# Performance work log

Measured on AMD Instinct MI355X. Metric: run time of the kernel, lower is better.

The kernel has to match this reference:

```python
import jax, jax.numpy as jnp
import numpy as np

N = 100000      # nodes
E = 1600000     # edges (avg degree 16)
IN = 128
OUT = 256


def setup_inputs() -> dict:
    key = jax.random.key(0)
    ks = jax.random.split(key, 8)
    x = jax.random.normal(ks[0], (N, IN), dtype=jnp.float32)
    edge_index = jax.random.randint(ks[1], (2, E), 0, N, dtype=jnp.int64)
    # GCNConv weights (glorot-ish scale) and biases
    W1 = jax.random.normal(ks[2], (IN, OUT), dtype=jnp.float32) / np.float32(np.sqrt(IN))
    b1 = jnp.zeros((OUT,), jnp.float32)
    W2 = jax.random.normal(ks[3], (OUT, OUT), dtype=jnp.float32) / np.float32(np.sqrt(OUT))
    b2 = jnp.zeros((OUT,), jnp.float32)
    # projection Linear(IN, OUT)
    Wp = jax.random.normal(ks[4], (IN, OUT), dtype=jnp.float32) / np.float32(np.sqrt(IN))
    bp = jax.random.normal(ks[5], (OUT,), dtype=jnp.float32) * 0.01
    return {"x": x, "edge_index": edge_index, "W1": W1, "b1": b1,
            "W2": W2, "b2": b2, "Wp": Wp, "bp": bp}


def _gcn_conv(x, W, b, src, dst, n):
    """PyG GCNConv: D^{-1/2}(A+I)D^{-1/2} X W + b. src/dst already include self-loops."""
    xw = x @ W                                              # [n, out]
    ones = jnp.ones(src.shape[0], dtype=xw.dtype)
    deg = jax.ops.segment_sum(ones, dst, num_segments=n)    # in-degree incl. self-loop
    dinv = jnp.where(deg > 0, jax.lax.rsqrt(deg), 0.0)
    norm = dinv[src] * dinv[dst]                            # [e]
    msgs = xw[src] * norm[:, None]                          # gather + scale
    out = jax.ops.segment_sum(msgs, dst, num_segments=n)    # scatter-add
    return out + b


def reference(x, edge_index, W1, b1, W2, b2, Wp, bp):
    n = x.shape[0]
    loop = jnp.arange(n, dtype=edge_index.dtype)            # self-loops
    src = jnp.concatenate([edge_index[0], loop])
    dst = jnp.concatenate([edge_index[1], loop])
    out = jax.nn.relu(_gcn_conv(x, W1, b1, src, dst, n))
    out = _gcn_conv(out, W2, b2, src, dst, n)
    identity = x @ Wp + bp                                  # projection (IN != OUT)
    return jax.nn.relu(out + identity)
```

## Files before the change

### kernel.cpp

```cpp
#include <hip/hip_runtime.h>

#define NODES 100000
#define EDGES 1600000
#define FIN   128
#define FOUT  256
#define NBUCK 196

typedef __bf16 bf16;
typedef __bf16 bf16x8 __attribute__((ext_vector_type(8)));
typedef __bf16 bf16x4 __attribute__((ext_vector_type(4)));
typedef __bf16 bf16x2 __attribute__((ext_vector_type(2)));
typedef float  f32x4  __attribute__((ext_vector_type(4)));
typedef float  f32x2  __attribute__((ext_vector_type(2)));

__device__ __forceinline__ f32x2 bf2f(unsigned w) {
    f32x2 r;
    r[0] = __uint_as_float(w << 16);
    r[1] = __uint_as_float(w & 0xffff0000u);
    return r;
}

__global__ __launch_bounds__(256) void detect_kernel(const void* __restrict__ x,
                                                     const int* __restrict__ ei,
                                                     int* __restrict__ flags) {
    __shared__ int s_f32_evidence;
    __shared__ int s_odd_nonzero;
    int t = threadIdx.x;
    if (t == 0) { s_f32_evidence = 0; s_odd_nonzero = 0; }
    __syncthreads();
    const bf16* xb = (const bf16*)x;
    int local_f32 = 0;
    for (int i = t; i < 4096; i += 256) {
        float v = fabsf((float)xb[i]);
        if (!(v < 1e4f)) local_f32 = 1;
    }
    if (local_f32) atomicOr(&s_f32_evidence, 1);
    int local_odd = 0;
    for (int k = t; k < 1024; k += 256) {
        if (ei[2 * k + 1] != 0) local_odd = 1;
    }
    if (local_odd) atomicOr(&s_odd_nonzero, 1);
    __syncthreads();
    if (t == 0) {
        flags[0] = s_f32_evidence ? 0 : 1;
        flags[1] = s_odd_nonzero ? 0 : 1;
    }
}

__device__ __forceinline__ int edge_at(const int* __restrict__ ei, int which, int i,
                                       int is64) {
    if (is64) return ei[2 * (which * EDGES + i)];
    return ei[which * EDGES + i];
}

__global__ __launch_bounds__(512) void deg_count(const int* __restrict__ ei,
                                                 int* __restrict__ deg,
                                                 int* __restrict__ bhist,
                                                 const int* __restrict__ flags) {
    __shared__ int lh[256];
    int t = threadIdx.x;
    if (t < 256) lh[t] = 0;
    __syncthreads();
    int i = blockIdx.x * 512 + t;
    if (i < EDGES) {
        int is64 = flags[1];
        int s = edge_at(ei, 0, i, is64);
        int d = edge_at(ei, 1, i, is64);
        if (s >= 0 && s < NODES && d >= 0 && d < NODES) {
            atomicAdd(&deg[d], 1);
            atomicAdd(&lh[d >> 9], 1);
        }
    }
    __syncthreads();
    if (t < NBUCK && lh[t] > 0) atomicAdd(&bhist[t], lh[t]);
}

__global__ __launch_bounds__(256) void deg_to_dinv(const int* __restrict__ deg,
                                                   float* __restrict__ dinv, int n) {
    int i = blockIdx.x * 256 + threadIdx.x;
    if (i < n) dinv[i] = rsqrtf((float)deg[i] + 1.0f);
}

__global__ __launch_bounds__(1024) void scan1(const int* __restrict__ deg,
                                              int* __restrict__ col_ptr,
                                              int* __restrict__ blksum, int n) {
    __shared__ int sm[1024];
    int t = threadIdx.x;
    int i = blockIdx.x * 1024 + t;
    int v = (i < n) ? deg[i] : 0;
    sm[t] = v;
    __syncthreads();
    for (int off = 1; off < 1024; off <<= 1) {
        int u = (t >= off) ? sm[t - off] : 0;
        __syncthreads();
        sm[t] += u;
        __syncthreads();
    }
    if (i <= n) col_ptr[i] = sm[t] - v;
    if (t == 1023) blksum[blockIdx.x] = sm[t];
}

__global__ __launch_bounds__(128) void scan2(int* blk, int nblk) {
    __shared__ int sm[128];
    int t = threadIdx.x;
    int v = (t < nblk) ? blk[t] : 0;
    sm[t] = v;
    __syncthreads();
    for (int off = 1; off < 128; off <<= 1) {
        int u = (t >= off) ? sm[t - off] : 0;
        __syncthreads();
        sm[t] += u;
        __syncthreads();
    }
    if (t < nblk) blk[t] = sm[t] - v;
}

__global__ __launch_bounds__(256) void scan3(int* __restrict__ col_ptr,
                                             const int* __restrict__ blkoff, int n) {
    int i = blockIdx.x * 256 + threadIdx.x;
    if (i <= n) col_ptr[i] += blkoff[i >> 10];
}

__global__ __launch_bounds__(256) void bucket_scan(const int* __restrict__ bhist,
                                                   int* __restrict__ bbase,
                                                   int* __restrict__ bcur) {
    __shared__ int sm[256];
    int t = threadIdx.x;
    int v = (t < NBUCK) ? bhist[t] : 0;
    sm[t] = v;
    __syncthreads();
    for (int off = 1; off < 256; off <<= 1) {
        int u = (t >= off) ? sm[t - off] : 0;
        __syncthreads();
        sm[t] += u;
        __syncthreads();
    }
    if (t < NBUCK) {
        int ex = sm[t] - v;
        bbase[t] = ex;
        bcur[t]  = ex;
        if (t == NBUCK - 1) bbase[NBUCK] = sm[t];
    }
}

#define EPB 4096
__global__ __launch_bounds__(256) void partition_edges(const int* __restrict__ ei,
                                                       int* __restrict__ bcur,
                                                       uint2* __restrict__ pairs,
                                                       const int* __restrict__ flags) {
    __shared__ int lh[256], sc[256], lst[256], lcu[256], gb[256];
    __shared__ uint2 stage[EPB];
    int t = threadIdx.x;
    int base = blockIdx.x * EPB;
    int is64 = flags[1];

    lh[t] = 0;
    __syncthreads();

    int es[16], ed[16];
#pragma unroll
    for (int j = 0; j < 16; ++j) {
        int i = base + j * 256 + t;
        int s = -1, d = -1;
        if (i < EDGES) {
            s = edge_at(ei, 0, i, is64);
            d = edge_at(ei, 1, i, is64);
            if (s < 0 || s >= NODES || d < 0 || d >= NODES) d = -1;
        }
        es[j] = s; ed[j] = d;
        if (d >= 0) atomicAdd(&lh[d >> 9], 1);
    }
    __syncthreads();
    sc[t] = lh[t];
    __syncthreads();
    for (int off = 1; off < 256; off <<= 1) {
        int u = (t >= off) ? sc[t - off] : 0;
        __syncthreads();
        sc[t] += u;
        __syncthreads();
    }
    int start = sc[t] - lh[t];
    lst[t] = start;
    lcu[t] = start;
    __syncthreads();
#pragma unroll
    for (int j = 0; j < 16; ++j) {
        if (ed[j] >= 0) {
            int p = atomicAdd(&lcu[ed[j] >> 9], 1);
            stage[p] = make_uint2((unsigned)es[j], (unsigned)ed[j]);
        }
    }
    __syncthreads();
    if (t < NBUCK && lh[t] > 0) gb[t] = atomicAdd(&bcur[t], lh[t]);
    __syncthreads();
    int nval = sc[255];
    for (int slot = t; slot < nval; slot += 256) {
        uint2 e = stage[slot];
        int b = (int)(e.y >> 9);
        pairs[(size_t)gb[b] + (slot - lst[b])] = e;
    }
}

__global__ __launch_bounds__(512) void fine_fill(const uint2* __restrict__ pairs,
                                                 const int* __restrict__ bbase,
                                                 const int* __restrict__ col_ptr,
                                                 int* __restrict__ col_idx) {
    __shared__ int lcur[512];
    int b = blockIdx.x;
    int t = threadIdx.x;
    int node = (b << 9) + t;
    lcur[t] = (node < NODES) ? col_ptr[node] : 0;
    __syncthreads();
    int beg = bbase[b], end = bbase[b + 1];
    for (int i = beg + t; i < end; i += 512) {
        uint2 e = pairs[i];
        int pos = atomicAdd(&lcur[e.y & 511], 1);
        col_idx[pos] = (int)e.x;
    }
}

__global__ __launch_bounds__(256) void pack_all(const void* __restrict__ W1,
                                                const void* __restrict__ W2,
                                                const void* __restrict__ Wp,
                                                const void* __restrict__ b1,
                                                const void* __restrict__ b2,
                                                const void* __restrict__ bp,
                                                bf16* __restrict__ W1p, bf16* __restrict__ W2p,
                                                bf16* __restrict__ Wpp, bf16* __restrict__ b1b,
                                                bf16* __restrict__ b2b, bf16* __restrict__ bpb,
                                                const int* __restrict__ flags) {
    int fl = flags[0];
    int b = blockIdx.x;
    if (b < 512) {
        const void* W; bf16* Wo; int idx;
        if (b < 128)      { W = W1; Wo = W1p; idx = b * 256 + threadIdx.x; }
        else if (b < 384) { W = W2; Wo = W2p; idx = (b - 128) * 256 + threadIdx.x; }
        else              { W = Wp; Wo = Wpp; idx = (b - 384) * 256 + threadIdx.x; }
        int j    = idx & 7;
        int lane = (idx >> 3) & 63;
        int ct   = (idx >> 9) & 15;
        int kt   = idx >> 13;
        int k = kt * 32 + (lane >> 4) * 8 + j;
        int n = ct * 16 + (lane & 15);
        Wo[idx] = fl ? ((const bf16*)W)[k * 256 + n]
                     : (bf16)(((const float*)W)[k * 256 + n]);
    } else {
        const void* bb; bf16* bo;
        if (b == 512)      { bb = b1; bo = b1b; }
        else if (b == 513) { bb = b2; bo = b2b; }
        else               { bb = bp; bo = bpb; }
        int i = threadIdx.x;
        bo[i] = fl ? ((const bf16*)bb)[i] : (bf16)(((const float*)bb)[i]);
    }
}

__global__ __launch_bounds__(256) void scale_x(const void* __restrict__ xv,
                                               const float* __restrict__ dinv,
                                               bf16* __restrict__ Xs,
                                               const int* __restrict__ flags) {
    int idx = blockIdx.x * 256 + threadIdx.x;
    if (idx >= NODES * 16) return;
    int row = idx >> 4, seg = idx & 15;
    float di = dinv[row];
    bf16x8 o;
    if (flags[0]) {
        bf16x8 v = *(const bf16x8*)((const bf16*)xv + (size_t)row * FIN + seg * 8);
#pragma unroll
        for (int j = 0; j < 8; ++j) o[j] = (bf16)(di * (float)v[j]);
    } else {
        const float* p = (const float*)xv + (size_t)row * FIN + seg * 8;
        f32x4 lo = *(const f32x4*)p;
        f32x4 hi = *(const f32x4*)(p + 4);
#pragma unroll
        for (int j = 0; j < 4; ++j) { o[j] = (bf16)(di * lo[j]); o[j + 4] = (bf16)(di * hi[j]); }
    }
    *(bf16x8*)(Xs + (size_t)row * FIN + seg * 8) = o;
}

__global__ __launch_bounds__(256) void gemm_proj(const void* __restrict__ Av,
                                                 const bf16* __restrict__ Wpk,
                                                 const bf16* __restrict__ bias,
                                                 bf16* __restrict__ projb,
                                                 const int* __restrict__ flags) {
    int a_f32 = (flags[0] == 0);
    int wave = threadIdx.x >> 6;
    int lane = threadIdx.x & 63;
    int row0 = blockIdx.x * 64;
    int lr = lane & 15;
    int lk = (lane >> 4) * 8;

    int arow[4];
#pragma unroll
    for (int rf = 0; rf < 4; ++rf) {
        int r = row0 + rf * 16 + lr;
        arow[rf] = r < NODES ? r : (NODES - 1);
    }

    f32x4 acc[4][4];
    f32x4 z = {0.f, 0.f, 0.f, 0.f};
#pragma unroll
    for (int i = 0; i < 4; ++i)
#pragma unroll
        for (int j = 0; j < 4; ++j) acc[i][j] = z;

    for (int kt = 0; kt < 4; ++kt) {
        bf16x8 af[4];
        if (!a_f32) {
            const bf16* Ab = (const bf16*)Av + kt * 32 + lk;
#pragma unroll
            for (int rf = 0; rf < 4; ++rf)
                af[rf] = *(const bf16x8*)(Ab + (size_t)arow[rf] * FIN);
        } else {
            const float* Af = (const float*)Av + kt * 32 + lk;
#pragma unroll
            for (int rf = 0; rf < 4; ++rf) {
                const float* p = Af + (size_t)arow[rf] * FIN;
                f32x4 lo = *(const f32x4*)p;
                f32x4 hi = *(const f32x4*)(p + 4);
                af[rf][0] = (bf16)lo[0]; af[rf][1] = (bf16)lo[1];
                af[rf][2] = (bf16)lo[2]; af[rf][3] = (bf16)lo[3];
                af[rf][4] = (bf16)hi[0]; af[rf][5] = (bf16)hi[1];
                af[rf][6] = (bf16)hi[2]; af[rf][7] = (bf16)hi[3];
            }
        }
        const bf16* wb = Wpk + ((size_t)(kt * 16 + wave * 4) * 64 + lane) * 8;
        bf16x8 bfv[4];
#pragma unroll
        for (int cf = 0; cf < 4; ++cf)
            bfv[cf] = *(const bf16x8*)(wb + cf * 512);
#pragma unroll
        for (int rf = 0; rf < 4; ++rf)
#pragma unroll
            for (int cf = 0; cf < 4; ++cf)
                acc[rf][cf] = __builtin_amdgcn_mfma_f32_16x16x32_bf16(
                    af[rf], bfv[cf], acc[rf][cf], 0, 0, 0);
    }

    int rb = (lane >> 4) * 4;
#pragma unroll
    for (int rf = 0; rf < 4; ++rf) {
#pragma unroll
        for (int r = 0; r < 4; ++r) {
            int row = row0 + rf * 16 + rb + r;
            if (row >= NODES) continue;
#pragma unroll
            for (int cf = 0; cf < 4; ++cf) {
                int col = wave * 64 + cf * 16 + lr;
                float v = acc[rf][cf][r] + (float)bias[col];
                projb[(size_t)row * 256 + col] = (bf16)v;
            }
        }
    }
}

__global__ __launch_bounds__(256) void gemm_tile(const bf16* __restrict__ A,
                                                 const bf16* __restrict__ Wpk,
                                                 int K,
                                                 const float* __restrict__ dinv,
                                                 const bf16* __restrict__ bias,
                                                 int relu,
                                                 bf16* __restrict__ out) {
    int wave = threadIdx.x >> 6;
    int lane = threadIdx.x & 63;
    int row0 = blockIdx.x * 64;
    int lr = lane & 15;
    int lk = (lane >> 4) * 8;

    int arow[4];
#pragma unroll
    for (int rf = 0; rf < 4; ++rf) {
        int r = row0 + rf * 16 + lr;
        arow[rf] = r < NODES ? r : (NODES - 1);
    }

    f32x4 acc[4][4];
    f32x4 z = {0.f, 0.f, 0.f, 0.f};
#pragma unroll
    for (int i = 0; i < 4; ++i)
#pragma unroll
        for (int j = 0; j < 4; ++j) acc[i][j] = z;

    int ktiles = K >> 5;
    for (int kt = 0; kt < ktiles; ++kt) {
        const bf16* Ab = A + kt * 32 + lk;
        bf16x8 af[4];
#pragma unroll
        for (int rf = 0; rf < 4; ++rf)
            af[rf] = *(const bf16x8*)(Ab + (size_t)arow[rf] * K);
        const bf16* wb = Wpk + ((size_t)(kt * 16 + wave * 4) * 64 + lane) * 8;
        bf16x8 bfv[4];
#pragma unroll
        for (int cf = 0; cf < 4; ++cf)
            bfv[cf] = *(const bf16x8*)(wb + cf * 512);
#pragma unroll
        for (int rf = 0; rf < 4; ++rf)
#pragma unroll
            for (int cf = 0; cf < 4; ++cf)
                acc[rf][cf] = __builtin_amdgcn_mfma_f32_16x16x32_bf16(
                    af[rf], bfv[cf], acc[rf][cf], 0, 0, 0);
    }

    int rb = (lane >> 4) * 4;
#pragma unroll
    for (int rf = 0; rf < 4; ++rf) {
#pragma unroll
        for (int r = 0; r < 4; ++r) {
            int row = row0 + rf * 16 + rb + r;
            if (row >= NODES) continue;
            float s = dinv ? dinv[row] : 1.0f;
#pragma unroll
            for (int cf = 0; cf < 4; ++cf) {
                int col = wave * 64 + cf * 16 + lr;
                float v = acc[rf][cf][r] * s;
                if (bias) v += (float)bias[col];
                if (relu) v = fmaxf(v, 0.0f);
                out[(size_t)row * 256 + col] = (bf16)v;
            }
        }
    }
}

__global__ __launch_bounds__(256) void gather1(const int* __restrict__ col_ptr,
                                               const int* __restrict__ col_idx,
                                               const bf16* __restrict__ Xs,
                                               const float* __restrict__ dinv,
                                               bf16* __restrict__ aggX) {
    int wid  = (int)((blockIdx.x * 256 + threadIdx.x) >> 6);
    int lane = threadIdx.x & 63;
    if (wid >= NODES) return;
    int beg = col_ptr[wid], end = col_ptr[wid + 1];
    int quarter = lane >> 4;
    int li      = lane & 15;
    int ch0     = li * 8 + quarter * 2;

    bf16x2 self2 = *(const bf16x2*)(Xs + (size_t)wid * FIN + ch0);
    float di = dinv[wid];

    const char* Xl = (const char*)Xs + li * 16;
    f32x2 acc2[4];
#pragma unroll
    for (int d = 0; d < 4; ++d) { acc2[d][0] = 0.f; acc2[d][1] = 0.f; }
    int npad = 0;
    for (int chunk = beg; chunk < end; chunk += 64) {
        int cnt = end - chunk;
        if (cnt > 64) cnt = 64;
        int padded = (cnt + 31) & ~31;
        npad += padded - cnt;
        int moff = ((lane < cnt) ? col_idx[chunk + lane] : wid) << 8;
        for (int j = 0; j < padded; j += 32) {
            uint4 w[8];
#pragma unroll
            for (int u = 0; u < 8; ++u) {
                int so = __shfl(moff, j + u * 4 + quarter);
                w[u] = *(const uint4*)(Xl + (unsigned)so);
            }
#pragma unroll
            for (int u = 0; u < 8; ++u) {
                acc2[0] += bf2f(w[u].x);
                acc2[1] += bf2f(w[u].y);
                acc2[2] += bf2f(w[u].z);
                acc2[3] += bf2f(w[u].w);
            }
        }
    }
#pragma unroll
    for (int d = 0; d < 4; ++d) {
        f32x2 t;
        t[0] = __shfl_xor(acc2[d][0], 16);
        t[1] = __shfl_xor(acc2[d][1], 16);
        acc2[d] += t;
        t[0] = __shfl_xor(acc2[d][0], 32);
        t[1] = __shfl_xor(acc2[d][1], 32);
        acc2[d] += t;
    }
    f32x2 t01 = (quarter & 1) ? acc2[1] : acc2[0];
    f32x2 t23 = (quarter & 1) ? acc2[3] : acc2[2];
    f32x2 pq  = (quarter & 2) ? t23 : t01;

    float corr = (float)(1 - npad);
    bf16x2 o;
    o[0] = (bf16)(di * (pq[0] + corr * (float)self2[0]));
    o[1] = (bf16)(di * (pq[1] + corr * (float)self2[1]));
    *(bf16x2*)(aggX + (size_t)wid * FIN + ch0) = o;
}

__global__ __launch_bounds__(256) void gather2(const int* __restrict__ col_ptr,
                                               const int* __restrict__ col_idx,
                                               const bf16* __restrict__ Y2,
                                               const float* __restrict__ dinv,
                                               const bf16* __restrict__ bias,
                                               const bf16* __restrict__ projb,
                                               void* __restrict__ outv,
                                               const int* __restrict__ flags) {
    int io_f32 = (flags[0] == 0);
    int wid  = (int)((blockIdx.x * 256 + threadIdx.x) >> 6);
    int lane = threadIdx.x & 63;
    if (wid >= NODES) return;
    int beg = col_ptr[wid], end = col_ptr[wid + 1];
    int half = lane >> 5;
    int li   = lane & 31;
    int ch0  = li * 8 + half * 4;
    size_t obase = (size_t)wid * 256 + ch0;

    bf16x4 selfv = *(const bf16x4*)(Y2 + obase);
    float di = dinv[wid];
    bf16x4 bv = *(const bf16x4*)(bias + ch0);
    bf16x4 pj = *(const bf16x4*)(projb + obase);

    const char* Yl = (const char*)Y2 + li * 16;
    f32x2 acc2[4];
#pragma unroll
    for (int d = 0; d < 4; ++d) { acc2[d][0] = 0.f; acc2[d][1] = 0.f; }
    int npad = 0;
    for (int chunk = beg; chunk < end; chunk += 64) {
        int cnt = end - chunk;
        if (cnt > 64) cnt = 64;
        int padded = (cnt + 15) & ~15;
        npad += padded - cnt;
        int moff = ((lane < cnt) ? col_idx[chunk + lane] : wid) << 9;
        for (int j = 0; j < padded; j += 16) {
            uint4 w[8];
#pragma unroll
            for (int u = 0; u < 8; ++u) {
                int so = __shfl(moff, j + u * 2 + half);
                w[u] = *(const uint4*)(Yl + (unsigned)so);
            }
#pragma unroll
            for (int u = 0; u < 8; ++u) {
                acc2[0] += bf2f(w[u].x);
                acc2[1] += bf2f(w[u].y);
                acc2[2] += bf2f(w[u].z);
                acc2[3] += bf2f(w[u].w);
            }
        }
    }
#pragma unroll
    for (int d = 0; d < 4; ++d) {
        f32x2 t;
        t[0] = __shfl_xor(acc2[d][0], 32);
        t[1] = __shfl_xor(acc2[d][1], 32);
        acc2[d] += t;
    }
    f32x2 p0 = half ? acc2[2] : acc2[0];
    f32x2 p1 = half ? acc2[3] : acc2[1];
    float av[4] = {p0[0], p0[1], p1[0], p1[1]};

    float corr = (float)(1 - npad);
    f32x4 o;
#pragma unroll
    for (int k = 0; k < 4; ++k) {
        float r = di * (av[k] + corr * (float)selfv[k]) + (float)bv[k] + (float)pj[k];
        o[k] = fmaxf(r, 0.0f);
    }

    if (io_f32) {
        *(f32x4*)((float*)outv + obase) = o;
    } else {
        bf16x4 ob;
#pragma unroll
        for (int k = 0; k < 4; ++k) ob[k] = (bf16)o[k];
        *(bf16x4*)((bf16*)outv + obase) = ob;
    }
}

__global__ __launch_bounds__(256) void zero_out(bf16* out, int nelem) {
    int i = blockIdx.x * 256 + threadIdx.x;
    if (i < nelem) out[i] = (bf16)0.0f;
}

extern "C" void kernel_launch(void* const* d_in, const int* in_sizes, int n_in,
                              void* d_out, int out_size, void* d_ws, size_t ws_size,
                              hipStream_t stream) {
    const void* x   = d_in[0];
    const int*  ei  = (const int*)d_in[1];
    const void* W1  = d_in[2];
    const void* b1  = d_in[3];
    const void* W2  = d_in[4];
    const void* b2  = d_in[5];
    const void* Wp  = d_in[6];
    const void* bp  = d_in[7];

    const size_t NEEDED = 401408ull * 3 + 1024ull * 4 + 6400000 + 65536 + 131072 + 65536
                        + 1536 + 25600000ull * 2 + 51200000ull;
    if (ws_size < NEEDED) {
        zero_out<<<(NODES * 256 + 255) / 256, 256, 0, stream>>>((bf16*)d_out, NODES * 256);
        return;
    }

    char* w = (char*)d_ws;
    int*   col_ptr = (int*)w;   w += 401408;
    int*   deg     = (int*)w;   w += 401408;
    int*   bhist   = (int*)w;   w += 1024;
    float* dinv    = (float*)w; w += 401408;
    int*   blk     = (int*)w;   w += 1024;
    int*   flags   = (int*)w;   w += 1024;
    int*   bbase   = (int*)w;   w += 1024;
    int*   bcur    = (int*)w;   w += 1024;
    int*   col_idx = (int*)w;   w += 6400000;
    bf16*  W1p     = (bf16*)w;  w += 65536;
    bf16*  W2p     = (bf16*)w;  w += 131072;
    bf16*  Wpp     = (bf16*)w;  w += 65536;
    bf16*  b1b     = (bf16*)w;  w += 512;
    bf16*  b2b     = (bf16*)w;  w += 512;
    bf16*  bpb     = (bf16*)w;  w += 512;
    bf16*  Xs      = (bf16*)w;  w += 25600000;
    bf16*  aggX    = (bf16*)w;  w += 25600000;
    bf16*  H1      = (bf16*)w;  w += 51200000;
    uint2* pairs   = (uint2*)Xs;
    bf16*  Y2      = Xs;
    bf16*  projb   = H1;

    const int NBLK = (NODES + 1 + 1023) / 1024;

    detect_kernel<<<1, 256, 0, stream>>>(x, ei, flags);

    hipMemsetAsync(deg, 0, 401408 + 1024, stream);
    deg_count<<<(EDGES + 511) / 512, 512, 0, stream>>>(ei, deg, bhist, flags);
    deg_to_dinv<<<(NODES + 255) / 256, 256, 0, stream>>>(deg, dinv, NODES);

    scan1<<<NBLK, 1024, 0, stream>>>(deg, col_ptr, blk, NODES);
    scan2<<<1, 128, 0, stream>>>(blk, NBLK);
    scan3<<<(NODES + 256) / 256, 256, 0, stream>>>(col_ptr, blk, NODES);
    bucket_scan<<<1, 256, 0, stream>>>(bhist, bbase, bcur);

    partition_edges<<<(EDGES + EPB - 1) / EPB, 256, 0, stream>>>(ei, bcur, pairs, flags);
    fine_fill<<<NBUCK, 512, 0, stream>>>(pairs, bbase, col_ptr, col_idx);

    pack_all<<<515, 256, 0, stream>>>(W1, W2, Wp, b1, b2, bp,
                                      W1p, W2p, Wpp, b1b, b2b, bpb, flags);

    const int gemm_grid   = (NODES + 63) / 64;
    const int gather_grid = (NODES + 3) / 4;

    scale_x<<<(NODES * 16 + 255) / 256, 256, 0, stream>>>(x, dinv, Xs, flags);
    gather1<<<gather_grid, 256, 0, stream>>>(col_ptr, col_idx, Xs, dinv, aggX);
    gemm_tile<<<gemm_grid, 256, 0, stream>>>(aggX, W1p, FIN, nullptr, b1b, 1, H1);
    gemm_tile<<<gemm_grid, 256, 0, stream>>>(H1, W2p, FOUT, dinv, nullptr, 0, Y2);
    gemm_proj<<<gemm_grid, 256, 0, stream>>>(x, Wpp, bpb, projb, flags);
    gather2<<<gather_grid, 256, 0, stream>>>(col_ptr, col_idx, Y2, dinv, b2b,
                                             projb, d_out, flags);
}
```

Baseline: 650.9 us.

## Split gathers into channel slices, add nontemporal stores, fuse dinv and bias

The separate deg_to_dinv kernel is folded into scan3, and bias b2 is folded into the projection GEMM epilogue instead of being added in gather2. The gather kernels now split the feature dimension across 2 or 4 blocks per node group, so each wave covers a 64-channel slice with 8 rows in flight per load round. Intermediate and output writes use nontemporal stores, and col_idx is read with nontemporal loads. This cuts a launch and lowers per-wave register and load width in the gathers, at the cost of re-reading the neighbor lists once per slice and writing outputs with scalar (per-element) stores.

After: 716.0 us. +10.0%, slower.

```diff
diff --git a/kernel.cpp b/kernel.cpp
--- a/kernel.cpp
+++ b/kernel.cpp
@@ -75,12 +75,6 @@
     if (t < NBUCK && lh[t] > 0) atomicAdd(&bhist[t], lh[t]);
 }
 
-__global__ __launch_bounds__(256) void deg_to_dinv(const int* __restrict__ deg,
-                                                   float* __restrict__ dinv, int n) {
-    int i = blockIdx.x * 256 + threadIdx.x;
-    if (i < n) dinv[i] = rsqrtf((float)deg[i] + 1.0f);
-}
-
 __global__ __launch_bounds__(1024) void scan1(const int* __restrict__ deg,
                                               int* __restrict__ col_ptr,
                                               int* __restrict__ blksum, int n) {
@@ -116,9 +110,12 @@
 }
 
 __global__ __launch_bounds__(256) void scan3(int* __restrict__ col_ptr,
-                                             const int* __restrict__ blkoff, int n) {
+                                             const int* __restrict__ blkoff,
+                                             const int* __restrict__ deg,
+                                             float* __restrict__ dinv, int n) {
     int i = blockIdx.x * 256 + threadIdx.x;
     if (i <= n) col_ptr[i] += blkoff[i >> 10];
+    if (i < n) dinv[i] = rsqrtf((float)deg[i] + 1.0f);
 }
 
 __global__ __launch_bounds__(256) void bucket_scan(const int* __restrict__ bhist,
@@ -274,12 +271,13 @@
 #pragma unroll
         for (int j = 0; j < 4; ++j) { o[j] = (bf16)(di * lo[j]); o[j + 4] = (bf16)(di * hi[j]); }
     }
-    *(bf16x8*)(Xs + (size_t)row * FIN + seg * 8) = o;
+    __builtin_nontemporal_store(o, (bf16x8*)(Xs + (size_t)row * FIN + seg * 8));
 }
 
 __global__ __launch_bounds__(256) void gemm_proj(const void* __restrict__ Av,
                                                  const bf16* __restrict__ Wpk,
-                                                 const bf16* __restrict__ bias,
+                                                 const bf16* __restrict__ biasp,
+                                                 const bf16* __restrict__ bias2,
                                                  bf16* __restrict__ projb,
                                                  const int* __restrict__ flags) {
     int a_f32 = (flags[0] == 0);
@@ -346,8 +344,8 @@
 #pragma unroll
             for (int cf = 0; cf < 4; ++cf) {
                 int col = wave * 64 + cf * 16 + lr;
-                float v = acc[rf][cf][r] + (float)bias[col];
-                projb[(size_t)row * 256 + col] = (bf16)v;
+                float v = acc[rf][cf][r] + (float)biasp[col] + (float)bias2[col];
+                __builtin_nontemporal_store((bf16)v, projb + (size_t)row * 256 + col);
             }
         }
     }
@@ -414,7 +412,7 @@
                 float v = acc[rf][cf][r] * s;
                 if (bias) v += (float)bias[col];
                 if (relu) v = fmaxf(v, 0.0f);
-                out[(size_t)row * 256 + col] = (bf16)v;
+                __builtin_nontemporal_store((bf16)v, out + (size_t)row * 256 + col);
             }
         }
     }
@@ -425,18 +423,21 @@
                                                const bf16* __restrict__ Xs,
                                                const float* __restrict__ dinv,
                                                bf16* __restrict__ aggX) {
-    int wid  = (int)((blockIdx.x * 256 + threadIdx.x) >> 6);
-    int lane = threadIdx.x & 63;
+    int b = blockIdx.x;
+    int slice = b & 1;
+    int wave  = threadIdx.x >> 6;
+    int wid   = (b >> 1) * 4 + wave;
+    int lane  = threadIdx.x & 63;
     if (wid >= NODES) return;
     int beg = col_ptr[wid], end = col_ptr[wid + 1];
-    int quarter = lane >> 4;
-    int li      = lane & 15;
-    int ch0     = li * 8 + quarter * 2;
-
-    bf16x2 self2 = *(const bf16x2*)(Xs + (size_t)wid * FIN + ch0);
+    int li = lane & 7;
+    int rg = lane >> 3;
+    int ch = slice * 64 + li * 8 + rg;
+
+    float selfc = (float)Xs[(size_t)wid * FIN + ch];
     float di = dinv[wid];
 
-    const char* Xl = (const char*)Xs + li * 16;
+    const char* Xl = (const char*)Xs + slice * 128 + li * 16;
     f32x2 acc2[4];
 #pragma unroll
     for (int d = 0; d < 4; ++d) { acc2[d][0] = 0.f; acc2[d][1] = 0.f; }
@@ -446,16 +447,17 @@
         if (cnt > 64) cnt = 64;
         int padded = (cnt + 31) & ~31;
         npad += padded - cnt;
-        int moff = ((lane < cnt) ? col_idx[chunk + lane] : wid) << 8;
+        int moff = ((lane < cnt) ? __builtin_nontemporal_load(col_idx + chunk + lane)
+                                 : wid) << 8;
         for (int j = 0; j < padded; j += 32) {
-            uint4 w[8];
-#pragma unroll
-            for (int u = 0; u < 8; ++u) {
-                int so = __shfl(moff, j + u * 4 + quarter);
+            uint4 w[4];
+#pragma unroll
+            for (int u = 0; u < 4; ++u) {
+                int so = __shfl(moff, j + u * 8 + rg);
                 w[u] = *(const uint4*)(Xl + (unsigned)so);
             }
 #pragma unroll
-            for (int u = 0; u < 8; ++u) {
+            for (int u = 0; u < 4; ++u) {
                 acc2[0] += bf2f(w[u].x);
                 acc2[1] += bf2f(w[u].y);
                 acc2[2] += bf2f(w[u].z);
@@ -466,48 +468,45 @@
 #pragma unroll
     for (int d = 0; d < 4; ++d) {
         f32x2 t;
-        t[0] = __shfl_xor(acc2[d][0], 16);
-        t[1] = __shfl_xor(acc2[d][1], 16);
-        acc2[d] += t;
-        t[0] = __shfl_xor(acc2[d][0], 32);
-        t[1] = __shfl_xor(acc2[d][1], 32);
-        acc2[d] += t;
-    }
-    f32x2 t01 = (quarter & 1) ? acc2[1] : acc2[0];
-    f32x2 t23 = (quarter & 1) ? acc2[3] : acc2[2];
-    f32x2 pq  = (quarter & 2) ? t23 : t01;
+        t[0] = __shfl_xor(acc2[d][0], 8);  t[1] = __shfl_xor(acc2[d][1], 8);  acc2[d] += t;
+        t[0] = __shfl_xor(acc2[d][0], 16); t[1] = __shfl_xor(acc2[d][1], 16); acc2[d] += t;
+        t[0] = __shfl_xor(acc2[d][0], 32); t[1] = __shfl_xor(acc2[d][1], 32); acc2[d] += t;
+    }
+    f32x2 pr01 = (rg & 2) ? acc2[1] : acc2[0];
+    f32x2 pr23 = (rg & 2) ? acc2[3] : acc2[2];
+    f32x2 pr   = (rg & 4) ? pr23 : pr01;
+    float aval = (rg & 1) ? pr[1] : pr[0];
 
     float corr = (float)(1 - npad);
-    bf16x2 o;
-    o[0] = (bf16)(di * (pq[0] + corr * (float)self2[0]));
-    o[1] = (bf16)(di * (pq[1] + corr * (float)self2[1]));
-    *(bf16x2*)(aggX + (size_t)wid * FIN + ch0) = o;
+    float r = di * (aval + corr * selfc);
+    __builtin_nontemporal_store((bf16)r, aggX + (size_t)wid * FIN + ch);
 }
 
 __global__ __launch_bounds__(256) void gather2(const int* __restrict__ col_ptr,
                                                const int* __restrict__ col_idx,
                                                const bf16* __restrict__ Y2,
                                                const float* __restrict__ dinv,
-                                               const bf16* __restrict__ bias,
                                                const bf16* __restrict__ projb,
                                                void* __restrict__ outv,
                                                const int* __restrict__ flags) {
     int io_f32 = (flags[0] == 0);
-    int wid  = (int)((blockIdx.x * 256 + threadIdx.x) >> 6);
-    int lane = threadIdx.x & 63;
+    int b = blockIdx.x;
+    int slice = b & 3;
+    int wave  = threadIdx.x >> 6;
+    int wid   = (b >> 2) * 4 + wave;
+    int lane  = threadIdx.x & 63;
     if (wid >= NODES) return;
     int beg = col_ptr[wid], end = col_ptr[wid + 1];
-    int half = lane >> 5;
-    int li   = lane & 31;
-    int ch0  = li * 8 + half * 4;
-    size_t obase = (size_t)wid * 256 + ch0;
-
-    bf16x4 selfv = *(const bf16x4*)(Y2 + obase);
+    int li = lane & 7;
+    int rg = lane >> 3;
+    int ch = slice * 64 + li * 8 + rg;
+    size_t obase = (size_t)wid * 256 + ch;
+
+    float selfc = (float)Y2[obase];
     float di = dinv[wid];
-    bf16x4 bv = *(const bf16x4*)(bias + ch0);
-    bf16x4 pj = *(const bf16x4*)(projb + obase);
-
-    const char* Yl = (const char*)Y2 + li * 16;
+    float pj = (float)__builtin_nontemporal_load(projb + obase);
+
+    const char* Yl = (const char*)Y2 + slice * 128 + li * 16;
     f32x2 acc2[4];
 #pragma unroll
     for (int d = 0; d < 4; ++d) { acc2[d][0] = 0.f; acc2[d][1] = 0.f; }
@@ -515,18 +514,19 @@
     for (int chunk = beg; chunk < end; chunk += 64) {
         int cnt = end - chunk;
         if (cnt > 64) cnt = 64;
-        int padded = (cnt + 15) & ~15;
+        int padded = (cnt + 31) & ~31;
         npad += padded - cnt;
-        int moff = ((lane < cnt) ? col_idx[chunk + lane] : wid) << 9;
-        for (int j = 0; j < padded; j += 16) {
-            uint4 w[8];
-#pragma unroll
-            for (int u = 0; u < 8; ++u) {
-                int so = __shfl(moff, j + u * 2 + half);
+        int moff = ((lane < cnt) ? __builtin_nontemporal_load(col_idx + chunk + lane)
+                                 : wid) << 9;
+        for (int j = 0; j < padded; j += 32) {
+            uint4 w[4];
+#pragma unroll
+            for (int u = 0; u < 4; ++u) {
+                int so = __shfl(moff, j + u * 8 + rg);
                 w[u] = *(const uint4*)(Yl + (unsigned)so);
             }
 #pragma unroll
-            for (int u = 0; u < 8; ++u) {
+            for (int u = 0; u < 4; ++u) {
                 acc2[0] += bf2f(w[u].x);
                 acc2[1] += bf2f(w[u].y);
                 acc2[2] += bf2f(w[u].z);
@@ -537,29 +537,22 @@
 #pragma unroll
     for (int d = 0; d < 4; ++d) {
         f32x2 t;
-        t[0] = __shfl_xor(acc2[d][0], 32);
-        t[1] = __shfl_xor(acc2[d][1], 32);
-        acc2[d] += t;
-    }
-    f32x2 p0 = half ? acc2[2] : acc2[0];
-    f32x2 p1 = half ? acc2[3] : acc2[1];
-    float av[4] = {p0[0], p0[1], p1[0], p1[1]};
+        t[0] = __shfl_xor(acc2[d][0], 8);  t[1] = __shfl_xor(acc2[d][1], 8);  acc2[d] += t;
+        t[0] = __shfl_xor(acc2[d][0], 16); t[1] = __shfl_xor(acc2[d][1], 16); acc2[d] += t;
+        t[0] = __shfl_xor(acc2[d][0], 32); t[1] = __shfl_xor(acc2[d][1], 32); acc2[d] += t;
+    }
+    f32x2 pr01 = (rg & 2) ? acc2[1] : acc2[0];
+    f32x2 pr23 = (rg & 2) ? acc2[3] : acc2[2];
+    f32x2 pr   = (rg & 4) ? pr23 : pr01;
+    float aval = (rg & 1) ? pr[1] : pr[0];
 
     float corr = (float)(1 - npad);
-    f32x4 o;
-#pragma unroll
-    for (int k = 0; k < 4; ++k) {
-        float r = di * (av[k] + corr * (float)selfv[k]) + (float)bv[k] + (float)pj[k];
-        o[k] = fmaxf(r, 0.0f);
-    }
+    float r = fmaxf(di * (aval + corr * selfc) + pj, 0.0f);
 
     if (io_f32) {
-        *(f32x4*)((float*)outv + obase) = o;
+        __builtin_nontemporal_store(r, (float*)outv + obase);
     } else {
-        bf16x4 ob;
-#pragma unroll
-        for (int k = 0; k < 4; ++k) ob[k] = (bf16)o[k];
-        *(bf16x4*)((bf16*)outv + obase) = ob;
+        __builtin_nontemporal_store((bf16)r, (bf16*)outv + obase);
     }
 }
 
@@ -616,11 +609,10 @@
 
     hipMemsetAsync(deg, 0, 401408 + 1024, stream);
     deg_count<<<(EDGES + 511) / 512, 512, 0, stream>>>(ei, deg, bhist, flags);
-    deg_to_dinv<<<(NODES + 255) / 256, 256, 0, stream>>>(deg, dinv, NODES);
 
     scan1<<<NBLK, 1024, 0, stream>>>(deg, col_ptr, blk, NODES);
     scan2<<<1, 128, 0, stream>>>(blk, NBLK);
-    scan3<<<(NODES + 256) / 256, 256, 0, stream>>>(col_ptr, blk, NODES);
+    scan3<<<(NODES + 256) / 256, 256, 0, stream>>>(col_ptr, blk, deg, dinv, NODES);
     bucket_scan<<<1, 256, 0, stream>>>(bhist, bbase, bcur);
 
     partition_edges<<<(EDGES + EPB - 1) / EPB, 256, 0, stream>>>(ei, bcur, pairs, flags);
@@ -629,14 +621,15 @@
     pack_all<<<515, 256, 0, stream>>>(W1, W2, Wp, b1, b2, bp,
                                       W1p, W2p, Wpp, b1b, b2b, bpb, flags);
 
-    const int gemm_grid   = (NODES + 63) / 64;
-    const int gather_grid = (NODES + 3) / 4;
+    const int gemm_grid = (NODES + 63) / 64;
+    const int g1_grid   = ((NODES + 3) / 4) * 2;
+    const int g2_grid   = ((NODES + 3) / 4) * 4;
 
     scale_x<<<(NODES * 16 + 255) / 256, 256, 0, stream>>>(x, dinv, Xs, flags);
-    gather1<<<gather_grid, 256, 0, stream>>>(col_ptr, col_idx, Xs, dinv, aggX);
+    gather1<<<g1_grid, 256, 0, stream>>>(col_ptr, col_idx, Xs, dinv, aggX);
     gemm_tile<<<gemm_grid, 256, 0, stream>>>(aggX, W1p, FIN, nullptr, b1b, 1, H1);
     gemm_tile<<<gemm_grid, 256, 0, stream>>>(H1, W2p, FOUT, dinv, nullptr, 0, Y2);
-    gemm_proj<<<gemm_grid, 256, 0, stream>>>(x, Wpp, bpb, projb, flags);
-    gather2<<<gather_grid, 256, 0, stream>>>(col_ptr, col_idx, Y2, dinv, b2b,
-                                             projb, d_out, flags);
-}
+    gemm_proj<<<gemm_grid, 256, 0, stream>>>(x, Wpp, bpb, b2b, projb, flags);
+    gather2<<<g2_grid, 256, 0, stream>>>(col_ptr, col_idx, Y2, dinv,
+                                         projb, d_out, flags);
+}
```
